# Performance work log

Hardware: AMD Instinct MI355X
Metric: run time of the kernel (lower is better)

Reference implementation:

```python
import jax, jax.numpy as jnp
import numpy as np

H = 64  # hidden_size

def _lstm_layer(x_tbf, W_ih, W_hh, b_ih, b_hh):
    # x_tbf: [T, B, F]; W_ih: [4H, F]; W_hh: [4H, H]; biases: [4H]
    T, B, _ = x_tbf.shape
    # precompute input projections for all timesteps at once: [T, B, 4H]
    x_proj = jnp.einsum('tbf,gf->tbg', x_tbf, W_ih) + (b_ih + b_hh)

    def step(carry, xp):
        h, c = carry
        gates = xp + h @ W_hh.T  # [B, 4H]
        i, f, g, o = jnp.split(gates, 4, axis=-1)
        i = jax.nn.sigmoid(i)
        f = jax.nn.sigmoid(f)
        g = jnp.tanh(g)
        o = jax.nn.sigmoid(o)
        c = f * c + i * g
        h = o * jnp.tanh(c)
        return (h, c), h

    h0 = jnp.zeros((B, H), dtype=x_tbf.dtype)
    c0 = jnp.zeros((B, H), dtype=x_tbf.dtype)
    (_, _), hs = jax.lax.scan(step, (h0, c0), x_proj)
    return hs  # [T, B, H]


def setup_inputs() -> dict:
    key = jax.random.key(0)
    ks = jax.random.split(key, 12)
    B, T, F = 1024, 512, 32
    s_in = 1.0 / np.sqrt(H)  # torch LSTM init scale
    u = lambda k, shape: jax.random.uniform(k, shape, jnp.float32, -s_in, s_in)
    return {
        'x': jax.random.normal(ks[0], (B, T, F), jnp.float32),
        'W_ih0': u(ks[1], (4 * H, F)),
        'W_hh0': u(ks[2], (4 * H, H)),
        'b_ih0': u(ks[3], (4 * H,)),
        'b_hh0': u(ks[4], (4 * H,)),
        'W_ih1': u(ks[5], (4 * H, H)),
        'W_hh1': u(ks[6], (4 * H, H)),
        'b_ih1': u(ks[7], (4 * H,)),
        'b_hh1': u(ks[8], (4 * H,)),
        'fc_w': u(ks[9], (1, H)),
        'fc_b': u(ks[10], (1,)),
    }


def reference(x, W_ih0, W_hh0, b_ih0, b_hh0, W_ih1, W_hh1, b_ih1, b_hh1, fc_w, fc_b):
    # x: [B, T, F] (batch_first); run 2 stacked LSTM layers, take last step, linear head
    x_tbf = jnp.transpose(x, (1, 0, 2))  # [T, B, F]
    h1 = _lstm_layer(x_tbf, W_ih0, W_hh0, b_ih0, b_hh0)  # [T, B, H]
    h2 = _lstm_layer(h1, W_ih1, W_hh1, b_ih1, b_hh1)      # [T, B, H]
    last = h2[-1]                                          # [B, H]
    return last @ fc_w.T + fc_b                            # [B, 1]
```

## Files before the change

kernel.cpp:

```cpp
#include <hip/hip_runtime.h>
#include <math.h>

#define H  64
#define F  32
#define NB 4
#define NT 512
#define HS 80
#define XS 40

typedef __attribute__((ext_vector_type(8))) short   s8v;
typedef __attribute__((ext_vector_type(8))) __bf16  bf8v;
typedef __attribute__((ext_vector_type(4))) float   f4v;

__device__ __forceinline__ unsigned short f2bf(float x) {
    unsigned u = __builtin_bit_cast(unsigned, x);
    u += 0x7FFFu + ((u >> 16) & 1u);
    return (unsigned short)(u >> 16);
}
__device__ __forceinline__ unsigned cvtpk(float a, float b) {
    unsigned r;
    asm volatile("v_cvt_pk_bf16_f32 %0, %1, %2" : "=v"(r) : "v"(a), "v"(b));
    return r;
}
__device__ __forceinline__ f4v mfma_(s8v a, s8v b, f4v c) {
    return __builtin_amdgcn_mfma_f32_16x16x32_bf16(
        __builtin_bit_cast(bf8v, a), __builtin_bit_cast(bf8v, b), c, 0, 0, 0);
}
__device__ __forceinline__ float sig_(float x) {
    return __builtin_amdgcn_rcpf(1.0f + __expf(-x));
}
__device__ __forceinline__ float tanh_(float x) {
    return 1.0f - 2.0f * __builtin_amdgcn_rcpf(1.0f + __expf(2.0f * x));
}

__device__ __forceinline__ s8v load_hi(const float* __restrict__ Wrow, int koff) {
    s8v hi;
    #pragma unroll
    for (int i = 0; i < 8; ++i) hi[i] = (short)f2bf(Wrow[koff + i]);
    return hi;
}

__global__ __launch_bounds__(NT, 2)
void lstm_v8(const float* __restrict__ x,
             const float* __restrict__ Wih0,
             const float* __restrict__ Whh0,
             const float* __restrict__ bih0,
             const float* __restrict__ bhh0,
             const float* __restrict__ Wih1,
             const float* __restrict__ Whh1,
             const float* __restrict__ bih1,
             const float* __restrict__ bhh1,
             const float* __restrict__ fcw,
             const float* __restrict__ fcb,
             float* __restrict__ out,
             int T, int B)
{
    const int tid  = threadIdx.x;
    const int w    = tid >> 6;
    const int wl   = w & 3;
    const bool isL0 = (w < 4);
    const int lane = tid & 63;
    const int j    = lane & 15;
    const int hi4  = lane >> 4;
    const int bm   = j >> 2;
    const int u    = 16 * wl + j;
    const int b0   = blockIdx.x * NB;

    __shared__ alignas(16) unsigned short xh[2][NB][XS];
    __shared__ alignas(16) unsigned short h0[2][NB][HS];
    __shared__ alignas(16) unsigned short h1[2][NB][HS];
    __shared__ float part[4][64];

    for (int i = tid; i < 2 * NB * HS; i += NT) {
        (&h0[0][0][0])[i] = 0;
        (&h1[0][0][0])[i] = 0;
    }

    if (isL0) {
        s8v wxh[4];
        s8v whh[4][2];
        float bias[4];
        #pragma unroll
        for (int g = 0; g < 4; ++g) {
            const int R = 64 * g + 16 * wl + j;
            wxh[g] = load_hi(&Wih0[R * F], 8 * hi4);
            #pragma unroll
            for (int kt = 0; kt < 2; ++kt)
                whh[g][kt] = load_hi(&Whh0[R * H], 32 * kt + 8 * hi4);
            bias[g] = bih0[R] + bhh0[R];
        }
        const bool stager = (tid < 128);
        const int xb = tid >> 5, xk = tid & 31;
        const float* xsrc = x + ((size_t)(b0 + xb) * T) * F + xk;
        float xpre = 0.f;
        if (stager) {
            const float v0 = xsrc[0];
            xh[0][xb][xk] = (unsigned short)cvtpk(v0, v0);
            if (T > 1) xpre = xsrc[F];
        }
        __syncthreads();

        float c = 0.f;
        #pragma unroll 1
        for (int s = 0; s <= T; ++s) {
            const int par = s & 1;
            if (s < T) {
                if (stager) {
                    if (s + 1 < T)
                        xh[par ^ 1][xb][xk] = (unsigned short)cvtpk(xpre, xpre);
                    if (s + 2 < T)
                        xpre = xsrc[(size_t)(s + 2) * F];
                }
                const s8v xfh = *(const s8v*)&xh[par][bm][8 * hi4];
                const s8v hf0 = *(const s8v*)&h0[par ^ 1][bm][8 * hi4];
                const s8v hf1 = *(const s8v*)&h0[par ^ 1][bm][8 * (4 + hi4)];

                f4v a[4], b[4];
                __builtin_amdgcn_s_setprio(1);
                #pragma unroll
                for (int g = 0; g < 4; ++g) {
                    f4v av = {bias[g], bias[g], bias[g], bias[g]};
                    a[g] = mfma_(xfh, wxh[g], av);
                    f4v bv = {0.f, 0.f, 0.f, 0.f};
                    bv = mfma_(hf0, whh[g][0], bv);
                    b[g] = mfma_(hf1, whh[g][1], bv);
                }
                __builtin_amdgcn_s_setprio(0);
                const float gi = sig_(a[0][0] + b[0][0]);
                const float gf = sig_(a[1][0] + b[1][0]);
                const float gg = tanh_(a[2][0] + b[2][0]);
                const float go = sig_(a[3][0] + b[3][0]);
                c = gf * c + gi * gg;
                const float hv = go * tanh_(c);
                h0[par][hi4][u] = (unsigned short)cvtpk(hv, hv);
            }
            __syncthreads();
        }
    } else {
        s8v wgh[4][2];
        s8v whh[4][2];
        float bias[4];
        #pragma unroll
        for (int g = 0; g < 4; ++g) {
            const int R = 64 * g + 16 * wl + j;
            #pragma unroll
            for (int kt = 0; kt < 2; ++kt) {
                wgh[g][kt] = load_hi(&Wih1[R * H], 32 * kt + 8 * hi4);
                whh[g][kt] = load_hi(&Whh1[R * H], 32 * kt + 8 * hi4);
            }
            bias[g] = bih1[R] + bhh1[R];
        }
        const float fcwr = fcw[u];
        __syncthreads();

        float c = 0.f;
        #pragma unroll 1
        for (int s = 0; s <= T; ++s) {
            const int par = s & 1;
            if (s >= 1) {
                const s8v gf0 = *(const s8v*)&h0[par ^ 1][bm][8 * hi4];
                const s8v gf1 = *(const s8v*)&h0[par ^ 1][bm][8 * (4 + hi4)];
                const s8v hf0 = *(const s8v*)&h1[par][bm][8 * hi4];
                const s8v hf1 = *(const s8v*)&h1[par][bm][8 * (4 + hi4)];

                f4v a[4], b[4];
                __builtin_amdgcn_s_setprio(1);
                #pragma unroll
                for (int g = 0; g < 4; ++g) {
                    f4v av = {bias[g], bias[g], bias[g], bias[g]};
                    av = mfma_(gf0, wgh[g][0], av);
                    a[g] = mfma_(gf1, wgh[g][1], av);
                    f4v bv = {0.f, 0.f, 0.f, 0.f};
                    bv = mfma_(hf0, whh[g][0], bv);
                    b[g] = mfma_(hf1, whh[g][1], bv);
                }
                __builtin_amdgcn_s_setprio(0);
                const float gi = sig_(a[0][0] + b[0][0]);
                const float gf = sig_(a[1][0] + b[1][0]);
                const float gg = tanh_(a[2][0] + b[2][0]);
                const float go = sig_(a[3][0] + b[3][0]);
                c = gf * c + gi * gg;
                const float hv = go * tanh_(c);
                if (s < T) {
                    h1[par ^ 1][hi4][u] = (unsigned short)cvtpk(hv, hv);
                } else {
                    part[wl][lane] = hv * fcwr;
                }
            }
            __syncthreads();
        }
    }

    if (tid < 64) {
        float v = part[0][lane] + part[1][lane] + part[2][lane] + part[3][lane];
        v += __shfl_xor(v, 1);
        v += __shfl_xor(v, 2);
        v += __shfl_xor(v, 4);
        v += __shfl_xor(v, 8);
        if (j == 0) out[b0 + hi4] = v + fcb[0];
    }
}

extern "C" void kernel_launch(void* const* d_in, const int* in_sizes, int n_in,
                              void* d_out, int out_size, void* d_ws, size_t ws_size,
                              hipStream_t stream) {
    const float* x    = (const float*)d_in[0];
    const float* Wih0 = (const float*)d_in[1];
    const float* Whh0 = (const float*)d_in[2];
    const float* bih0 = (const float*)d_in[3];
    const float* bhh0 = (const float*)d_in[4];
    const float* Wih1 = (const float*)d_in[5];
    const float* Whh1 = (const float*)d_in[6];
    const float* bih1 = (const float*)d_in[7];
    const float* bhh1 = (const float*)d_in[8];
    const float* fcw  = (const float*)d_in[9];
    const float* fcb  = (const float*)d_in[10];
    float* out = (float*)d_out;

    const int B = out_size;
    const int T = in_sizes[0] / (B * F);

    dim3 grid(B / NB), block(NT);
    hipLaunchKernelGGL(lstm_v8, grid, block, 0, stream,
                       x, Wih0, Whh0, bih0, bhh0,
                       Wih1, Whh1, bih1, bhh1, fcw, fcb,
                       out, T, B);
}
```

Measured before the change: 234.2 us.

## Load x directly into registers and use lighter LDS-only barriers with 2x unroll

Removes the shared-memory x staging buffer: each layer-0 lane now loads its own 8 input features straight from global memory into registers, double-buffered two steps ahead, and packs them to bf16 in place. The per-step __syncthreads is replaced by an lgkmcnt(0) wait plus s_barrier, so the barrier no longer waits on outstanding global loads. The time loop is unrolled by two so the parity index is a compile-time constant. The aim is less LDS traffic and a shorter critical path through each step's barrier. The cost is more redundant global loads of x (each lane loads x instead of 128 stagers), and the code assumes T is even.

```diff
diff --git a/kernel.cpp b/kernel.cpp
--- a/kernel.cpp
+++ b/kernel.cpp
@@ -6,7 +6,6 @@
 #define NB 4
 #define NT 512
 #define HS 80
-#define XS 40
 
 typedef __attribute__((ext_vector_type(8))) short   s8v;
 typedef __attribute__((ext_vector_type(8))) __bf16  bf8v;
@@ -19,7 +18,7 @@
 }
 __device__ __forceinline__ unsigned cvtpk(float a, float b) {
     unsigned r;
-    asm volatile("v_cvt_pk_bf16_f32 %0, %1, %2" : "=v"(r) : "v"(a), "v"(b));
+    asm("v_cvt_pk_bf16_f32 %0, %1, %2" : "=v"(r) : "v"(a), "v"(b));
     return r;
 }
 __device__ __forceinline__ f4v mfma_(s8v a, s8v b, f4v c) {
@@ -31,6 +30,10 @@
 }
 __device__ __forceinline__ float tanh_(float x) {
     return 1.0f - 2.0f * __builtin_amdgcn_rcpf(1.0f + __expf(2.0f * x));
+}
+__device__ __forceinline__ void bar_lds() {
+    asm volatile("s_waitcnt lgkmcnt(0)" ::: "memory");
+    __builtin_amdgcn_s_barrier();
 }
 
 __device__ __forceinline__ s8v load_hi(const float* __restrict__ Wrow, int koff) {
@@ -41,7 +44,7 @@
 }
 
 __global__ __launch_bounds__(NT, 2)
-void lstm_v8(const float* __restrict__ x,
+void lstm_v9(const float* __restrict__ x,
              const float* __restrict__ Wih0,
              const float* __restrict__ Whh0,
              const float* __restrict__ bih0,
@@ -66,7 +69,6 @@
     const int u    = 16 * wl + j;
     const int b0   = blockIdx.x * NB;
 
-    __shared__ alignas(16) unsigned short xh[2][NB][XS];
     __shared__ alignas(16) unsigned short h0[2][NB][HS];
     __shared__ alignas(16) unsigned short h1[2][NB][HS];
     __shared__ float part[4][64];
@@ -89,53 +91,56 @@
                 whh[g][kt] = load_hi(&Whh0[R * H], 32 * kt + 8 * hi4);
             bias[g] = bih0[R] + bhh0[R];
         }
-        const bool stager = (tid < 128);
-        const int xb = tid >> 5, xk = tid & 31;
-        const float* xsrc = x + ((size_t)(b0 + xb) * T) * F + xk;
-        float xpre = 0.f;
-        if (stager) {
-            const float v0 = xsrc[0];
-            xh[0][xb][xk] = (unsigned short)cvtpk(v0, v0);
-            if (T > 1) xpre = xsrc[F];
-        }
+        const float* xrow = x + ((size_t)(b0 + bm) * T) * F + 8 * hi4;
+        float4 xA0 = *(const float4*)(xrow);
+        float4 xA1 = *(const float4*)(xrow + 4);
+        float4 xB0 = *(const float4*)(xrow + F);
+        float4 xB1 = *(const float4*)(xrow + F + 4);
+
         __syncthreads();
 
         float c = 0.f;
+        auto stepL0 = [&](int s, int par, float4& xr0, float4& xr1) {
+            s8v xf;
+            unsigned* xfu = (unsigned*)&xf;
+            xfu[0] = cvtpk(xr0.x, xr0.y);
+            xfu[1] = cvtpk(xr0.z, xr0.w);
+            xfu[2] = cvtpk(xr1.x, xr1.y);
+            xfu[3] = cvtpk(xr1.z, xr1.w);
+            const size_t tld = (size_t)((s + 2 < T) ? (s + 2) : (T - 1)) * F;
+            xr0 = *(const float4*)(xrow + tld);
+            xr1 = *(const float4*)(xrow + tld + 4);
+
+            const s8v hf0 = *(const s8v*)&h0[par ^ 1][bm][8 * hi4];
+            const s8v hf1 = *(const s8v*)&h0[par ^ 1][bm][8 * (4 + hi4)];
+
+            f4v a[4], b[4];
+            __builtin_amdgcn_s_setprio(1);
+            #pragma unroll
+            for (int g = 0; g < 4; ++g) {
+                f4v av = {bias[g], bias[g], bias[g], bias[g]};
+                a[g] = mfma_(xf, wxh[g], av);
+                f4v bv = {0.f, 0.f, 0.f, 0.f};
+                bv = mfma_(hf0, whh[g][0], bv);
+                b[g] = mfma_(hf1, whh[g][1], bv);
+            }
+            __builtin_amdgcn_s_setprio(0);
+            const float gi = sig_(a[0][0] + b[0][0]);
+            const float gf = sig_(a[1][0] + b[1][0]);
+            const float gg = tanh_(a[2][0] + b[2][0]);
+            const float go = sig_(a[3][0] + b[3][0]);
+            c = gf * c + gi * gg;
+            const float hv = go * tanh_(c);
+            h0[par][hi4][u] = (unsigned short)cvtpk(hv, hv);
+            bar_lds();
+        };
+
         #pragma unroll 1
-        for (int s = 0; s <= T; ++s) {
-            const int par = s & 1;
-            if (s < T) {
-                if (stager) {
-                    if (s + 1 < T)
-                        xh[par ^ 1][xb][xk] = (unsigned short)cvtpk(xpre, xpre);
-                    if (s + 2 < T)
-                        xpre = xsrc[(size_t)(s + 2) * F];
-                }
-                const s8v xfh = *(const s8v*)&xh[par][bm][8 * hi4];
-                const s8v hf0 = *(const s8v*)&h0[par ^ 1][bm][8 * hi4];
-                const s8v hf1 = *(const s8v*)&h0[par ^ 1][bm][8 * (4 + hi4)];
-
-                f4v a[4], b[4];
-                __builtin_amdgcn_s_setprio(1);
-                #pragma unroll
-                for (int g = 0; g < 4; ++g) {
-                    f4v av = {bias[g], bias[g], bias[g], bias[g]};
-                    a[g] = mfma_(xfh, wxh[g], av);
-                    f4v bv = {0.f, 0.f, 0.f, 0.f};
-                    bv = mfma_(hf0, whh[g][0], bv);
-                    b[g] = mfma_(hf1, whh[g][1], bv);
-                }
-                __builtin_amdgcn_s_setprio(0);
-                const float gi = sig_(a[0][0] + b[0][0]);
-                const float gf = sig_(a[1][0] + b[1][0]);
-                const float gg = tanh_(a[2][0] + b[2][0]);
-                const float go = sig_(a[3][0] + b[3][0]);
-                c = gf * c + gi * gg;
-                const float hv = go * tanh_(c);
-                h0[par][hi4][u] = (unsigned short)cvtpk(hv, hv);
-            }
-            __syncthreads();
-        }
+        for (int s = 0; s < T; s += 2) {
+            stepL0(s,     0, xA0, xA1);
+            stepL0(s + 1, 1, xB0, xB1);
+        }
+        bar_lds();
     } else {
         s8v wgh[4][2];
         s8v whh[4][2];
@@ -154,9 +159,7 @@
         __syncthreads();
 
         float c = 0.f;
-        #pragma unroll 1
-        for (int s = 0; s <= T; ++s) {
-            const int par = s & 1;
+        auto stepL1 = [&](int s, int par) {
             if (s >= 1) {
                 const s8v gf0 = *(const s8v*)&h0[par ^ 1][bm][8 * hi4];
                 const s8v gf1 = *(const s8v*)&h0[par ^ 1][bm][8 * (4 + hi4)];
@@ -187,9 +190,18 @@
                     part[wl][lane] = hv * fcwr;
                 }
             }
-            __syncthreads();
-        }
+            bar_lds();
+        };
+
+        #pragma unroll 1
+        for (int s = 0; s < T; s += 2) {
+            stepL1(s,     0);
+            stepL1(s + 1, 1);
+        }
+        stepL1(T, 0);
     }
+
+    __syncthreads();
 
     if (tid < 64) {
         float v = part[0][lane] + part[1][lane] + part[2][lane] + part[3][lane];
@@ -221,7 +233,7 @@
     const int T = in_sizes[0] / (B * F);
 
     dim3 grid(B / NB), block(NT);
-    hipLaunchKernelGGL(lstm_v8, grid, block, 0, stream,
+    hipLaunchKernelGGL(lstm_v9, grid, block, 0, stream,
                        x, Wih0, Whh0, bih0, bhh0,
                        Wih1, Whh1, bih1, bhh1, fcw, fcb,
                        out, T, B);
```

New measurement: 210.4 us. -10.2%, faster.

## Offload input projections to a third warp group to shorten recurrent critical path

Applied to the files above, without the earlier changes.

Adds a third group of four waves that computes the layer-0 input projection (x·Wih0+bias) and the layer-1 input projection (h0·Wih1+bias) one step ahead, writing them to shared-memory ring buffers. The two recurrent groups then only do the hidden-state MFMAs, so each step's serial chain is shorter. Layer 1 is skewed by an extra step, and __syncthreads is replaced by a waitcnt plus raw barrier. This costs more threads per block (768, three blocks per CU), extra LDS traffic and a longer pipeline.

```diff
diff --git a/kernel.cpp b/kernel.cpp
--- a/kernel.cpp
+++ b/kernel.cpp
@@ -4,9 +4,8 @@
 #define H  64
 #define F  32
 #define NB 4
-#define NT 512
+#define NT 768
 #define HS 80
-#define XS 40
 
 typedef __attribute__((ext_vector_type(8))) short   s8v;
 typedef __attribute__((ext_vector_type(8))) __bf16  bf8v;
@@ -19,7 +18,7 @@
 }
 __device__ __forceinline__ unsigned cvtpk(float a, float b) {
     unsigned r;
-    asm volatile("v_cvt_pk_bf16_f32 %0, %1, %2" : "=v"(r) : "v"(a), "v"(b));
+    asm("v_cvt_pk_bf16_f32 %0, %1, %2" : "=v"(r) : "v"(a), "v"(b));
     return r;
 }
 __device__ __forceinline__ f4v mfma_(s8v a, s8v b, f4v c) {
@@ -32,33 +31,42 @@
 __device__ __forceinline__ float tanh_(float x) {
     return 1.0f - 2.0f * __builtin_amdgcn_rcpf(1.0f + __expf(2.0f * x));
 }
-
+__device__ __forceinline__ void bar_lds() {
+    asm volatile("s_waitcnt lgkmcnt(0)" ::: "memory");
+    __builtin_amdgcn_s_barrier();
+}
 __device__ __forceinline__ s8v load_hi(const float* __restrict__ Wrow, int koff) {
     s8v hi;
     #pragma unroll
     for (int i = 0; i < 8; ++i) hi[i] = (short)f2bf(Wrow[koff + i]);
     return hi;
 }
-
-__global__ __launch_bounds__(NT, 2)
-void lstm_v8(const float* __restrict__ x,
-             const float* __restrict__ Wih0,
-             const float* __restrict__ Whh0,
-             const float* __restrict__ bih0,
-             const float* __restrict__ bhh0,
-             const float* __restrict__ Wih1,
-             const float* __restrict__ Whh1,
-             const float* __restrict__ bih1,
-             const float* __restrict__ bhh1,
-             const float* __restrict__ fcw,
-             const float* __restrict__ fcb,
-             float* __restrict__ out,
-             int T, int B)
+__device__ __forceinline__ s8v xfrag(const float4& a, const float4& b) {
+    s8v r; unsigned* ru = (unsigned*)&r;
+    ru[0] = cvtpk(a.x, a.y); ru[1] = cvtpk(a.z, a.w);
+    ru[2] = cvtpk(b.x, b.y); ru[3] = cvtpk(b.z, b.w);
+    return r;
+}
+
+__global__ __launch_bounds__(NT, 3)
+void lstm_v10(const float* __restrict__ x,
+              const float* __restrict__ Wih0,
+              const float* __restrict__ Whh0,
+              const float* __restrict__ bih0,
+              const float* __restrict__ bhh0,
+              const float* __restrict__ Wih1,
+              const float* __restrict__ Whh1,
+              const float* __restrict__ bih1,
+              const float* __restrict__ bhh1,
+              const float* __restrict__ fcw,
+              const float* __restrict__ fcb,
+              float* __restrict__ out,
+              int T, int B)
 {
     const int tid  = threadIdx.x;
     const int w    = tid >> 6;
     const int wl   = w & 3;
-    const bool isL0 = (w < 4);
+    const int grp  = w >> 2;
     const int lane = tid & 63;
     const int j    = lane & 15;
     const int hi4  = lane >> 4;
@@ -66,9 +74,10 @@
     const int u    = 16 * wl + j;
     const int b0   = blockIdx.x * NB;
 
-    __shared__ alignas(16) unsigned short xh[2][NB][XS];
     __shared__ alignas(16) unsigned short h0[2][NB][HS];
     __shared__ alignas(16) unsigned short h1[2][NB][HS];
+    __shared__ float XP[3][4][H][NB];
+    __shared__ float P1[2][4][H][NB];
     __shared__ float part[4][64];
 
     for (int i = tid; i < 2 * NB * HS; i += NT) {
@@ -76,120 +85,164 @@
         (&h1[0][0][0])[i] = 0;
     }
 
-    if (isL0) {
-        s8v wxh[4];
+    if (grp == 0) {
         s8v whh[4][2];
-        float bias[4];
         #pragma unroll
         for (int g = 0; g < 4; ++g) {
             const int R = 64 * g + 16 * wl + j;
-            wxh[g] = load_hi(&Wih0[R * F], 8 * hi4);
-            #pragma unroll
-            for (int kt = 0; kt < 2; ++kt)
-                whh[g][kt] = load_hi(&Whh0[R * H], 32 * kt + 8 * hi4);
-            bias[g] = bih0[R] + bhh0[R];
-        }
-        const bool stager = (tid < 128);
-        const int xb = tid >> 5, xk = tid & 31;
-        const float* xsrc = x + ((size_t)(b0 + xb) * T) * F + xk;
-        float xpre = 0.f;
-        if (stager) {
-            const float v0 = xsrc[0];
-            xh[0][xb][xk] = (unsigned short)cvtpk(v0, v0);
-            if (T > 1) xpre = xsrc[F];
+            whh[g][0] = load_hi(&Whh0[R * H], 8 * hi4);
+            whh[g][1] = load_hi(&Whh0[R * H], 32 + 8 * hi4);
         }
         __syncthreads();
 
         float c = 0.f;
+        int s0 = 0;
         #pragma unroll 1
-        for (int s = 0; s <= T; ++s) {
+        for (int s = 0; s <= T + 1; ++s) {
             const int par = s & 1;
             if (s < T) {
-                if (stager) {
-                    if (s + 1 < T)
-                        xh[par ^ 1][xb][xk] = (unsigned short)cvtpk(xpre, xpre);
-                    if (s + 2 < T)
-                        xpre = xsrc[(size_t)(s + 2) * F];
-                }
-                const s8v xfh = *(const s8v*)&xh[par][bm][8 * hi4];
                 const s8v hf0 = *(const s8v*)&h0[par ^ 1][bm][8 * hi4];
                 const s8v hf1 = *(const s8v*)&h0[par ^ 1][bm][8 * (4 + hi4)];
-
-                f4v a[4], b[4];
+                float xp[4];
+                #pragma unroll
+                for (int g = 0; g < 4; ++g) xp[g] = XP[s0][g][u][hi4];
+                f4v acc[4];
                 __builtin_amdgcn_s_setprio(1);
                 #pragma unroll
                 for (int g = 0; g < 4; ++g) {
-                    f4v av = {bias[g], bias[g], bias[g], bias[g]};
-                    a[g] = mfma_(xfh, wxh[g], av);
-                    f4v bv = {0.f, 0.f, 0.f, 0.f};
-                    bv = mfma_(hf0, whh[g][0], bv);
-                    b[g] = mfma_(hf1, whh[g][1], bv);
+                    f4v av = {xp[g], xp[g], xp[g], xp[g]};
+                    av = mfma_(hf0, whh[g][0], av);
+                    acc[g] = mfma_(hf1, whh[g][1], av);
                 }
                 __builtin_amdgcn_s_setprio(0);
-                const float gi = sig_(a[0][0] + b[0][0]);
-                const float gf = sig_(a[1][0] + b[1][0]);
-                const float gg = tanh_(a[2][0] + b[2][0]);
-                const float go = sig_(a[3][0] + b[3][0]);
+                const float gi = sig_(acc[0][0]);
+                const float gf = sig_(acc[1][0]);
+                const float gg = tanh_(acc[2][0]);
+                const float go = sig_(acc[3][0]);
                 c = gf * c + gi * gg;
                 const float hv = go * tanh_(c);
                 h0[par][hi4][u] = (unsigned short)cvtpk(hv, hv);
             }
-            __syncthreads();
-        }
-    } else {
-        s8v wgh[4][2];
+            s0 = (s0 == 2) ? 0 : s0 + 1;
+            bar_lds();
+        }
+    } else if (grp == 1) {
         s8v whh[4][2];
-        float bias[4];
         #pragma unroll
         for (int g = 0; g < 4; ++g) {
             const int R = 64 * g + 16 * wl + j;
-            #pragma unroll
-            for (int kt = 0; kt < 2; ++kt) {
-                wgh[g][kt] = load_hi(&Wih1[R * H], 32 * kt + 8 * hi4);
-                whh[g][kt] = load_hi(&Whh1[R * H], 32 * kt + 8 * hi4);
-            }
-            bias[g] = bih1[R] + bhh1[R];
+            whh[g][0] = load_hi(&Whh1[R * H], 8 * hi4);
+            whh[g][1] = load_hi(&Whh1[R * H], 32 + 8 * hi4);
         }
         const float fcwr = fcw[u];
         __syncthreads();
 
         float c = 0.f;
         #pragma unroll 1
-        for (int s = 0; s <= T; ++s) {
+        for (int s = 0; s <= T + 1; ++s) {
             const int par = s & 1;
-            if (s >= 1) {
-                const s8v gf0 = *(const s8v*)&h0[par ^ 1][bm][8 * hi4];
-                const s8v gf1 = *(const s8v*)&h0[par ^ 1][bm][8 * (4 + hi4)];
-                const s8v hf0 = *(const s8v*)&h1[par][bm][8 * hi4];
-                const s8v hf1 = *(const s8v*)&h1[par][bm][8 * (4 + hi4)];
-
-                f4v a[4], b[4];
+            if (s >= 2) {
+                const s8v hf0 = *(const s8v*)&h1[par ^ 1][bm][8 * hi4];
+                const s8v hf1 = *(const s8v*)&h1[par ^ 1][bm][8 * (4 + hi4)];
+                float p[4];
+                #pragma unroll
+                for (int g = 0; g < 4; ++g) p[g] = P1[par][g][u][hi4];
+                f4v acc[4];
                 __builtin_amdgcn_s_setprio(1);
                 #pragma unroll
                 for (int g = 0; g < 4; ++g) {
-                    f4v av = {bias[g], bias[g], bias[g], bias[g]};
-                    av = mfma_(gf0, wgh[g][0], av);
-                    a[g] = mfma_(gf1, wgh[g][1], av);
-                    f4v bv = {0.f, 0.f, 0.f, 0.f};
-                    bv = mfma_(hf0, whh[g][0], bv);
-                    b[g] = mfma_(hf1, whh[g][1], bv);
+                    f4v av = {p[g], p[g], p[g], p[g]};
+                    av = mfma_(hf0, whh[g][0], av);
+                    acc[g] = mfma_(hf1, whh[g][1], av);
                 }
                 __builtin_amdgcn_s_setprio(0);
-                const float gi = sig_(a[0][0] + b[0][0]);
-                const float gf = sig_(a[1][0] + b[1][0]);
-                const float gg = tanh_(a[2][0] + b[2][0]);
-                const float go = sig_(a[3][0] + b[3][0]);
+                const float gi = sig_(acc[0][0]);
+                const float gf = sig_(acc[1][0]);
+                const float gg = tanh_(acc[2][0]);
+                const float go = sig_(acc[3][0]);
                 c = gf * c + gi * gg;
                 const float hv = go * tanh_(c);
-                if (s < T) {
-                    h1[par ^ 1][hi4][u] = (unsigned short)cvtpk(hv, hv);
+                if (s <= T) {
+                    h1[par][hi4][u] = (unsigned short)cvtpk(hv, hv);
                 } else {
                     part[wl][lane] = hv * fcwr;
                 }
             }
-            __syncthreads();
+            bar_lds();
+        }
+    } else {
+        s8v wx[4], wg1[4][2];
+        float b0g[4], b1g[4];
+        #pragma unroll
+        for (int g = 0; g < 4; ++g) {
+            const int R = 64 * g + 16 * wl + j;
+            wx[g] = load_hi(&Wih0[R * F], 8 * hi4);
+            wg1[g][0] = load_hi(&Wih1[R * H], 8 * hi4);
+            wg1[g][1] = load_hi(&Wih1[R * H], 32 + 8 * hi4);
+            b0g[g] = bih0[R] + bhh0[R];
+            b1g[g] = bih1[R] + bhh1[R];
+        }
+        const float* xrow = x + ((size_t)(b0 + bm) * T) * F + 8 * hi4;
+        const int tmax = T - 1;
+        {
+            const float4 p00 = *(const float4*)(xrow);
+            const float4 p01 = *(const float4*)(xrow + 4);
+            const size_t o1 = (size_t)((1 < tmax) ? 1 : tmax) * F;
+            const float4 p10 = *(const float4*)(xrow + o1);
+            const float4 p11 = *(const float4*)(xrow + o1 + 4);
+            const s8v xf0 = xfrag(p00, p01);
+            const s8v xf1 = xfrag(p10, p11);
+            #pragma unroll
+            for (int g = 0; g < 4; ++g) {
+                f4v av = {b0g[g], b0g[g], b0g[g], b0g[g]};
+                f4v a = mfma_(xf0, wx[g], av);
+                XP[0][g][u][hi4] = a[0];
+                f4v bv = {b0g[g], b0g[g], b0g[g], b0g[g]};
+                f4v b = mfma_(xf1, wx[g], bv);
+                XP[1][g][u][hi4] = b[0];
+            }
+        }
+        const size_t o2 = (size_t)((2 < tmax) ? 2 : tmax) * F;
+        const size_t o3 = (size_t)((3 < tmax) ? 3 : tmax) * F;
+        float4 xA0 = *(const float4*)(xrow + o2), xA1 = *(const float4*)(xrow + o2 + 4);
+        float4 xB0 = *(const float4*)(xrow + o3), xB1 = *(const float4*)(xrow + o3 + 4);
+        __syncthreads();
+
+        int slot2 = 2;
+        #pragma unroll 1
+        for (int s = 0; s <= T + 1; ++s) {
+            const int par = s & 1;
+            if (s >= 1 && s <= T) {
+                const s8v hf0 = *(const s8v*)&h0[par ^ 1][bm][8 * hi4];
+                const s8v hf1 = *(const s8v*)&h0[par ^ 1][bm][8 * (4 + hi4)];
+                #pragma unroll
+                for (int g = 0; g < 4; ++g) {
+                    f4v av = {b1g[g], b1g[g], b1g[g], b1g[g]};
+                    av = mfma_(hf0, wg1[g][0], av);
+                    f4v a = mfma_(hf1, wg1[g][1], av);
+                    P1[par ^ 1][g][u][hi4] = a[0];
+                }
+            }
+            if (s + 2 < T) {
+                float4& r0 = (s & 1) ? xB0 : xA0;
+                float4& r1 = (s & 1) ? xB1 : xA1;
+                const s8v xf = xfrag(r0, r1);
+                #pragma unroll
+                for (int g = 0; g < 4; ++g) {
+                    f4v av = {b0g[g], b0g[g], b0g[g], b0g[g]};
+                    f4v a = mfma_(xf, wx[g], av);
+                    XP[slot2][g][u][hi4] = a[0];
+                }
+                const size_t tld = (size_t)((s + 4 < tmax) ? (s + 4) : tmax) * F;
+                r0 = *(const float4*)(xrow + tld);
+                r1 = *(const float4*)(xrow + tld + 4);
+            }
+            slot2 = (slot2 == 2) ? 0 : slot2 + 1;
+            bar_lds();
         }
     }
+
+    __syncthreads();
 
     if (tid < 64) {
         float v = part[0][lane] + part[1][lane] + part[2][lane] + part[3][lane];
@@ -221,7 +274,7 @@
     const int T = in_sizes[0] / (B * F);
 
     dim3 grid(B / NB), block(NT);
-    hipLaunchKernelGGL(lstm_v8, grid, block, 0, stream,
+    hipLaunchKernelGGL(lstm_v10, grid, block, 0, stream,
                        x, Wih0, Whh0, bih0, bhh0,
                        Wih1, Whh1, bih1, bhh1, fcw, fcb,
                        out, T, B);
```

Result: slower. 443.8 us (+89.4%).
